# Kernel optimization log

Measured on AMD Instinct MI355X. Metric: run time of the kernel, lower is better.

Reference implementation:

```python
import jax, jax.numpy as jnp
import numpy as np

B, S, E = 16, 2048, 1024

def setup_inputs() -> dict:
    key = jax.random.key(0)
    ks = jax.random.split(key, 7)
    scale = 1.0 / np.sqrt(E)
    x = jax.random.normal(ks[0], (B, S, E), dtype=jnp.float32)
    wq = jax.random.normal(ks[1], (E, E), dtype=jnp.float32) * scale
    bq = jax.random.normal(ks[2], (E,), dtype=jnp.float32) * 0.01
    wk = jax.random.normal(ks[3], (E, E), dtype=jnp.float32) * scale
    bk = jax.random.normal(ks[4], (E,), dtype=jnp.float32) * 0.01
    wv = jax.random.normal(ks[5], (E, E), dtype=jnp.float32) * scale
    bv = jax.random.normal(ks[6], (E,), dtype=jnp.float32) * 0.01
    return {"x": x, "wq": wq, "bq": bq, "wk": wk, "bk": bk, "wv": wv, "bv": bv}

def reference(x, wq, bq, wk, bk, wv, bv):
    # Linear layers: y = x @ W^T + b (torch nn.Linear convention)
    Q = jnp.einsum('bse,fe->bsf', x, wq) + bq
    K = jnp.einsum('bse,fe->bsf', x, wk) + bk
    V = jnp.einsum('bse,fe->bsf', x, wv) + bv
    scale = 1.0 / jnp.sqrt(jnp.asarray(x.shape[-1], dtype=x.dtype))
    score = jnp.einsum('bqe,bke->bqk', Q, K) * scale  # [B,S,S]
    attn = jax.nn.softmax(score, axis=-1)
    # dropout is identity in eval mode
    context = jnp.einsum('bqk,bke->bqe', attn, V)  # [B,S,E]
    return jnp.mean(context, axis=1)  # [B,E]
```

## Files before the change

### kernel.cpp

```cpp
#include <hip/hip_runtime.h>


#define B_ 16
#define S_ 2048
#define E_ 1024

typedef __bf16 bf16x8 __attribute__((ext_vector_type(8)));
typedef float f32x4 __attribute__((ext_vector_type(4)));

__device__ __forceinline__ unsigned short f2bf(float f) {
  unsigned int u = __float_as_uint(f);
  u = (u + 0x7FFFu + ((u >> 16) & 1u)) >> 16;
  return (unsigned short)u;
}
__device__ __forceinline__ float bf2f(unsigned short u) {
  return __uint_as_float((unsigned int)u << 16);
}

__global__ __launch_bounds__(256) void gvec_kernel(
    const float* __restrict__ wk, const float* __restrict__ bq,
    float* __restrict__ g) {
  const int e = blockIdx.x * 256 + threadIdx.x;
  const int f0 = blockIdx.y * 32;
  float acc = 0.f;
#pragma unroll
  for (int i = 0; i < 32; ++i) acc += wk[(size_t)(f0 + i) * E_ + e] * bq[f0 + i];
  atomicAdd(&g[e], acc);
}

__global__ __launch_bounds__(256) void cast_x_v_kernel(
    const float* __restrict__ x, const float* __restrict__ g,
    unsigned short* __restrict__ xbf, float* __restrict__ vs) {
  const int row = blockIdx.x, t = threadIdx.x;
  const size_t i = (size_t)row * E_ + t * 4;
  float4 v = *(const float4*)(x + i);
  float4 gv = *(const float4*)(g + t * 4);
  ushort4 o;
  o.x = f2bf(v.x); o.y = f2bf(v.y); o.z = f2bf(v.z); o.w = f2bf(v.w);
  *(ushort4*)(xbf + i) = o;
  float p = v.x * gv.x + v.y * gv.y + v.z * gv.z + v.w * gv.w;
#pragma unroll
  for (int off = 32; off >= 1; off >>= 1) p += __shfl_xor(p, off);
  __shared__ float wsp[4];
  if ((t & 63) == 0) wsp[t >> 6] = p;
  __syncthreads();
  if (t == 0) vs[row] = (wsp[0] + wsp[1] + wsp[2] + wsp[3]) * 0.03125f;
}

__global__ __launch_bounds__(256) void tcast_kernel(
    const float* __restrict__ src, unsigned short* __restrict__ dst) {
  __shared__ float tile[32][33];
  const int tx = threadIdx.x & 31, ty = threadIdx.x >> 5;
  const int f0 = blockIdx.y * 32, e0 = blockIdx.x * 32;
#pragma unroll
  for (int j = 0; j < 4; ++j)
    tile[ty + 8 * j][tx] = src[(size_t)(f0 + ty + 8 * j) * E_ + e0 + tx];
  __syncthreads();
#pragma unroll
  for (int j = 0; j < 4; ++j)
    dst[(size_t)(e0 + ty + 8 * j) * E_ + f0 + tx] = f2bf(tile[tx][ty + 8 * j]);
}

template <int MODE>
__global__ __launch_bounds__(256, 2) void gemm_bt(
    const unsigned short* __restrict__ A, const unsigned short* __restrict__ Bm,
    unsigned short* __restrict__ Cout, const float* __restrict__ bias,
    float* __restrict__ rowsum, float scale,
    int K, int lda, int ldb, int ldc,
    long long strideA, long long strideB, long long strideC) {
  __shared__ unsigned short As[128 * 64];
  __shared__ unsigned short Bs[128 * 64];

  const int tid = threadIdx.x;
  const int wave = tid >> 6;
  const int lane = tid & 63;
  const int bz = blockIdx.z;
  const unsigned short* Ab = A + (size_t)bz * strideA;
  const unsigned short* Bb = Bm + (size_t)bz * strideB;
  const int rowBase = blockIdx.y * 128;
  const int colBase = blockIdx.x * 128;

  const int waveM = wave >> 1, waveN = wave & 1;
  const int lrow = lane & 15, lq = lane >> 4;

  const int rsub = lane >> 3;
  const int gOff = (((lane & 7) ^ rsub) << 3);

  f32x4 acc[4][4];
#pragma unroll
  for (int i = 0; i < 4; ++i)
#pragma unroll
    for (int j = 0; j < 4; ++j) {
      f32x4 z = {0.f, 0.f, 0.f, 0.f};
      acc[i][j] = z;
    }

  for (int k0 = 0; k0 < K; k0 += 64) {
#pragma unroll
    for (int i = 0; i < 4; ++i) {
      const int chunk = wave * 4 + i;
      const int r = chunk * 8 + rsub;
      const unsigned short* ga = Ab + (size_t)(rowBase + r) * lda + (k0 + gOff);
      const unsigned short* gb = Bb + (size_t)(colBase + r) * ldb + (k0 + gOff);
      __builtin_amdgcn_global_load_lds(
          (const __attribute__((address_space(1))) void*)ga,
          (__attribute__((address_space(3))) void*)(&As[chunk * 512]), 16, 0, 0);
      __builtin_amdgcn_global_load_lds(
          (const __attribute__((address_space(1))) void*)gb,
          (__attribute__((address_space(3))) void*)(&Bs[chunk * 512]), 16, 0, 0);
    }
    __syncthreads();

#pragma unroll
    for (int ks = 0; ks < 2; ++ks) {
      const int gg = (((ks * 4 + lq) ^ (lrow & 7)) << 3);
      bf16x8 af[4], bfv[4];
#pragma unroll
      for (int mi = 0; mi < 4; ++mi)
        af[mi] = *(const bf16x8*)(&As[(waveM * 64 + mi * 16 + lrow) * 64 + gg]);
#pragma unroll
      for (int ni = 0; ni < 4; ++ni)
        bfv[ni] = *(const bf16x8*)(&Bs[(waveN * 64 + ni * 16 + lrow) * 64 + gg]);
#pragma unroll
      for (int mi = 0; mi < 4; ++mi)
#pragma unroll
        for (int ni = 0; ni < 4; ++ni)
          acc[mi][ni] = __builtin_amdgcn_mfma_f32_16x16x32_bf16(
              af[mi], bfv[ni], acc[mi][ni], 0, 0, 0);
    }
    __syncthreads();
  }

  unsigned short* Cb = Cout + (size_t)bz * strideC;
  if constexpr (MODE == 0) {
#pragma unroll
    for (int mi = 0; mi < 4; ++mi) {
      const int grow = rowBase + waveM * 64 + mi * 16 + lq * 4;
#pragma unroll
      for (int ni = 0; ni < 4; ++ni) {
        const int gcol = colBase + waveN * 64 + ni * 16 + lrow;
        const float badd = bias ? bias[gcol] : 0.f;
#pragma unroll
        for (int r = 0; r < 4; ++r)
          Cb[(size_t)(grow + r) * ldc + gcol] =
              f2bf(acc[mi][ni][r] * scale + badd);
      }
    }
  } else {
    float* rs = rowsum + (size_t)bz * S_;
    const float* vsb = bias + (size_t)bz * S_;
#pragma unroll
    for (int mi = 0; mi < 4; ++mi) {
      const int grow = rowBase + waveM * 64 + mi * 16 + lq * 4;
#pragma unroll
      for (int r = 0; r < 4; ++r) {
        float partial = 0.f;
#pragma unroll
        for (int ni = 0; ni < 4; ++ni) {
          const int gcol = colBase + waveN * 64 + ni * 16 + lrow;
          const float e = __expf(acc[mi][ni][r] * scale + vsb[gcol]);
          Cb[(size_t)(grow + r) * ldc + gcol] = f2bf(e);
          partial += e;
        }
        partial += __shfl_xor(partial, 1);
        partial += __shfl_xor(partial, 2);
        partial += __shfl_xor(partial, 4);
        partial += __shfl_xor(partial, 8);
        if (lrow == 0) atomicAdd(&rs[grow + r], partial);
      }
    }
  }
}

__global__ __launch_bounds__(256) void colsum_kernel(
    const unsigned int* __restrict__ Epk, const float* __restrict__ rowsum,
    float* __restrict__ wsum) {
  const int b = blockIdx.y, q0 = blockIdx.x * 128, t = threadIdx.x;
  __shared__ float rinv[128];
  if (t < 128) rinv[t] = 1.0f / rowsum[(size_t)b * S_ + q0 + t];
  __syncthreads();
  float cs0[4] = {0, 0, 0, 0}, cs1[4] = {0, 0, 0, 0};
  const unsigned int* Eb = Epk + ((size_t)b * S_ + q0) * (S_ / 2);
  for (int q = 0; q < 128; ++q) {
    const float rv = rinv[q];
    const unsigned int* row = Eb + (size_t)q * (S_ / 2);
#pragma unroll
    for (int j = 0; j < 4; ++j) {
      const unsigned int p = row[t + 256 * j];
      cs0[j] += bf2f((unsigned short)(p & 0xFFFF)) * rv;
      cs1[j] += bf2f((unsigned short)(p >> 16)) * rv;
    }
  }
  const float inv = 1.0f / (float)S_;
#pragma unroll
  for (int j = 0; j < 4; ++j) {
    atomicAdd(&wsum[(size_t)b * S_ + 2 * (t + 256 * j)], cs0[j] * inv);
    atomicAdd(&wsum[(size_t)b * S_ + 2 * (t + 256 * j) + 1], cs1[j] * inv);
  }
}

__global__ __launch_bounds__(256) void xbar_kernel(
    const float* __restrict__ x, const float* __restrict__ wsum,
    float* __restrict__ xbar) {
  const int b = blockIdx.y, kc = blockIdx.x, t = threadIdx.x;
  float acc[4] = {0, 0, 0, 0};
  for (int k0 = 0; k0 < 256; ++k0) {
    const int k = kc * 256 + k0;
    const float w = wsum[(size_t)b * S_ + k];
    const float* xr = x + ((size_t)b * S_ + k) * E_;
#pragma unroll
    for (int c = 0; c < 4; ++c) acc[c] += w * xr[c * 256 + t];
  }
#pragma unroll
  for (int c = 0; c < 4; ++c)
    atomicAdd(&xbar[(size_t)b * E_ + c * 256 + t], acc[c]);
}

__global__ __launch_bounds__(256) void out_kernel(
    const float* __restrict__ xbar, const float* __restrict__ wv,
    const float* __restrict__ bv, float* __restrict__ out) {
  const int gid = blockIdx.x * 256 + threadIdx.x;
  const int b = gid >> 10, e = gid & 1023;
  const float4* xr = (const float4*)(xbar + (size_t)b * E_);
  const float4* wr = (const float4*)(wv + (size_t)e * E_);
  float s = 0.f;
  for (int j = 0; j < E_ / 4; ++j) {
    float4 a = xr[j], w = wr[j];
    s += a.x * w.x + a.y * w.y + a.z * w.z + a.w * w.w;
  }
  out[gid] = s + bv[e];
}

extern "C" void kernel_launch(void* const* d_in, const int* in_sizes, int n_in,
                              void* d_out, int out_size, void* d_ws,
                              size_t ws_size, hipStream_t stream) {
  const float* x = (const float*)d_in[0];
  const float* wq = (const float*)d_in[1];
  const float* bq = (const float*)d_in[2];
  const float* wk = (const float*)d_in[3];
  const float* wv = (const float*)d_in[5];
  const float* bv = (const float*)d_in[6];
  float* out = (float*)d_out;

  char* ws = (char*)d_ws;
  const size_t MB = 1ull << 20;
  unsigned short* xbf = (unsigned short*)(ws);
  unsigned short* y = (unsigned short*)(ws + 64 * MB);
  unsigned short* Ebuf = (unsigned short*)(ws + 128 * MB);
  unsigned short* WqT = (unsigned short*)(ws + 256 * MB);
  unsigned short* WkT = (unsigned short*)(ws + 258 * MB);
  unsigned short* Mt = (unsigned short*)(ws + 260 * MB);
  float* g = (float*)(ws + 262 * MB);
  float* rowsum = g + E_;
  float* wsum = rowsum + B_ * S_;
  float* xbar = wsum + B_ * S_;
  float* vs = xbar + B_ * E_;

  hipMemsetAsync(g, 0, (size_t)(E_ + 2 * B_ * S_ + B_ * E_) * sizeof(float),
                 stream);

  gvec_kernel<<<dim3(E_ / 256, 32), 256, 0, stream>>>(wk, bq, g);
  cast_x_v_kernel<<<B_ * S_, 256, 0, stream>>>(x, g, xbf, vs);
  tcast_kernel<<<dim3(32, 32), 256, 0, stream>>>(wq, WqT);
  tcast_kernel<<<dim3(32, 32), 256, 0, stream>>>(wk, WkT);

  gemm_bt<0><<<dim3(8, 8), 256, 0, stream>>>(
      WkT, WqT, Mt, nullptr, nullptr, 1.0f, E_, E_, E_, E_, 0, 0, 0);
  gemm_bt<0><<<dim3(E_ / 128, (B_ * S_) / 128), 256, 0, stream>>>(
      xbf, Mt, y, nullptr, nullptr, 1.0f, E_, E_, E_, E_, 0, 0, 0);
  gemm_bt<1><<<dim3(S_ / 128, S_ / 128, B_), 256, 0, stream>>>(
      y, xbf, Ebuf, vs, rowsum, 0.03125f, E_, E_, E_, S_,
      (long long)S_ * E_, (long long)S_ * E_, (long long)S_ * S_);

  colsum_kernel<<<dim3(S_ / 128, B_), 256, 0, stream>>>(
      (const unsigned int*)Ebuf, rowsum, wsum);
  xbar_kernel<<<dim3(S_ / 256, B_), 256, 0, stream>>>(x, wsum, xbar);
  out_kernel<<<(B_ * E_) / 256, 256, 0, stream>>>(xbar, wv, bv, out);
}
```

Measured before the change: 580.3 us.

## Store softmax exponentials as packed fp8 and split xbar/out reductions wider

The unnormalized attention exponentials are now stored as fp8 (packed four per 32-bit word, with a permuted column order) instead of bf16. This halves the 64 MB-per-batch E buffer traffic written by the score GEMM and read by the column-sum kernel, and the column-sum indexing is changed to match the new packing. The xbar kernel now uses float4 loads and more blocks. The output GEMV is split over four K-chunks using atomics on a zeroed output. The fp8 format risks accuracy loss in the attention weights, and the extra atomics add contention.

```diff
diff --git a/kernel.cpp b/kernel.cpp
--- a/kernel.cpp
+++ b/kernel.cpp
@@ -7,14 +7,12 @@
 
 typedef __bf16 bf16x8 __attribute__((ext_vector_type(8)));
 typedef float f32x4 __attribute__((ext_vector_type(4)));
+typedef float f32x2 __attribute__((ext_vector_type(2)));
 
 __device__ __forceinline__ unsigned short f2bf(float f) {
   unsigned int u = __float_as_uint(f);
   u = (u + 0x7FFFu + ((u >> 16) & 1u)) >> 16;
   return (unsigned short)u;
-}
-__device__ __forceinline__ float bf2f(unsigned short u) {
-  return __uint_as_float((unsigned int)u << 16);
 }
 
 __global__ __launch_bounds__(256) void gvec_kernel(
@@ -64,7 +62,7 @@
 template <int MODE>
 __global__ __launch_bounds__(256, 2) void gemm_bt(
     const unsigned short* __restrict__ A, const unsigned short* __restrict__ Bm,
-    unsigned short* __restrict__ Cout, const float* __restrict__ bias,
+    void* __restrict__ Cout, const float* __restrict__ bias,
     float* __restrict__ rowsum, float scale,
     int K, int lda, int ldb, int ldc,
     long long strideA, long long strideB, long long strideC) {
@@ -131,8 +129,8 @@
     __syncthreads();
   }
 
-  unsigned short* Cb = Cout + (size_t)bz * strideC;
   if constexpr (MODE == 0) {
+    unsigned short* Cb = (unsigned short*)Cout + (size_t)bz * strideC;
 #pragma unroll
     for (int mi = 0; mi < 4; ++mi) {
       const int grow = rowBase + waveM * 64 + mi * 16 + lq * 4;
@@ -147,21 +145,30 @@
       }
     }
   } else {
+    unsigned char* Eb = (unsigned char*)Cout + (size_t)bz * strideC;
     float* rs = rowsum + (size_t)bz * S_;
     const float* vsb = bias + (size_t)bz * S_;
+    float badd[4];
+#pragma unroll
+    for (int ni = 0; ni < 4; ++ni)
+      badd[ni] = vsb[colBase + waveN * 64 + ni * 16 + lrow];
 #pragma unroll
     for (int mi = 0; mi < 4; ++mi) {
       const int grow = rowBase + waveM * 64 + mi * 16 + lq * 4;
 #pragma unroll
       for (int r = 0; r < 4; ++r) {
+        float e[4];
         float partial = 0.f;
 #pragma unroll
         for (int ni = 0; ni < 4; ++ni) {
-          const int gcol = colBase + waveN * 64 + ni * 16 + lrow;
-          const float e = __expf(acc[mi][ni][r] * scale + vsb[gcol]);
-          Cb[(size_t)(grow + r) * ldc + gcol] = f2bf(e);
-          partial += e;
+          e[ni] = __expf(acc[mi][ni][r] * scale + badd[ni]);
+          partial += e[ni];
         }
+        unsigned int pk = 0;
+        pk = __builtin_amdgcn_cvt_pk_fp8_f32(e[0], e[1], pk, false);
+        pk = __builtin_amdgcn_cvt_pk_fp8_f32(e[2], e[3], pk, true);
+        *(unsigned int*)(&Eb[(size_t)(grow + r) * S_ + colBase + waveN * 64 +
+                             lrow * 4]) = pk;
         partial += __shfl_xor(partial, 1);
         partial += __shfl_xor(partial, 2);
         partial += __shfl_xor(partial, 4);
@@ -175,27 +182,34 @@
 __global__ __launch_bounds__(256) void colsum_kernel(
     const unsigned int* __restrict__ Epk, const float* __restrict__ rowsum,
     float* __restrict__ wsum) {
-  const int b = blockIdx.y, q0 = blockIdx.x * 128, t = threadIdx.x;
-  __shared__ float rinv[128];
-  if (t < 128) rinv[t] = 1.0f / rowsum[(size_t)b * S_ + q0 + t];
+  const int b = blockIdx.y, q0 = blockIdx.x * 64, t = threadIdx.x;
+  __shared__ float rinv[64];
+  if (t < 64) rinv[t] = 1.0f / rowsum[(size_t)b * S_ + q0 + t];
   __syncthreads();
-  float cs0[4] = {0, 0, 0, 0}, cs1[4] = {0, 0, 0, 0};
-  const unsigned int* Eb = Epk + ((size_t)b * S_ + q0) * (S_ / 2);
-  for (int q = 0; q < 128; ++q) {
+  float cs[2][4] = {{0, 0, 0, 0}, {0, 0, 0, 0}};
+  const unsigned int* Eb = Epk + ((size_t)b * S_ + q0) * (S_ / 4);
+  for (int q = 0; q < 64; ++q) {
     const float rv = rinv[q];
-    const unsigned int* row = Eb + (size_t)q * (S_ / 2);
-#pragma unroll
-    for (int j = 0; j < 4; ++j) {
+    const unsigned int* row = Eb + (size_t)q * (S_ / 4);
+#pragma unroll
+    for (int j = 0; j < 2; ++j) {
       const unsigned int p = row[t + 256 * j];
-      cs0[j] += bf2f((unsigned short)(p & 0xFFFF)) * rv;
-      cs1[j] += bf2f((unsigned short)(p >> 16)) * rv;
+      f32x2 lo = __builtin_amdgcn_cvt_pk_f32_fp8(p, false);
+      f32x2 hi = __builtin_amdgcn_cvt_pk_f32_fp8(p, true);
+      cs[j][0] += lo[0] * rv;
+      cs[j][1] += lo[1] * rv;
+      cs[j][2] += hi[0] * rv;
+      cs[j][3] += hi[1] * rv;
     }
   }
   const float inv = 1.0f / (float)S_;
 #pragma unroll
-  for (int j = 0; j < 4; ++j) {
-    atomicAdd(&wsum[(size_t)b * S_ + 2 * (t + 256 * j)], cs0[j] * inv);
-    atomicAdd(&wsum[(size_t)b * S_ + 2 * (t + 256 * j) + 1], cs1[j] * inv);
+  for (int j = 0; j < 2; ++j) {
+    const int d = t + 256 * j;
+    const int base = (d >> 4) * 64 + (d & 15);
+#pragma unroll
+    for (int jj = 0; jj < 4; ++jj)
+      atomicAdd(&wsum[(size_t)b * S_ + base + 16 * jj], cs[j][jj] * inv);
   }
 }
 
@@ -203,17 +217,19 @@
     const float* __restrict__ x, const float* __restrict__ wsum,
     float* __restrict__ xbar) {
   const int b = blockIdx.y, kc = blockIdx.x, t = threadIdx.x;
-  float acc[4] = {0, 0, 0, 0};
-  for (int k0 = 0; k0 < 256; ++k0) {
-    const int k = kc * 256 + k0;
+  float4 acc = {0.f, 0.f, 0.f, 0.f};
+  for (int k0 = 0; k0 < 128; ++k0) {
+    const int k = kc * 128 + k0;
     const float w = wsum[(size_t)b * S_ + k];
-    const float* xr = x + ((size_t)b * S_ + k) * E_;
-#pragma unroll
-    for (int c = 0; c < 4; ++c) acc[c] += w * xr[c * 256 + t];
-  }
-#pragma unroll
-  for (int c = 0; c < 4; ++c)
-    atomicAdd(&xbar[(size_t)b * E_ + c * 256 + t], acc[c]);
+    const float4 xv = *(const float4*)(x + ((size_t)b * S_ + k) * E_ + t * 4);
+    acc.x += w * xv.x; acc.y += w * xv.y;
+    acc.z += w * xv.z; acc.w += w * xv.w;
+  }
+  float* xb = xbar + (size_t)b * E_ + t * 4;
+  atomicAdd(&xb[0], acc.x);
+  atomicAdd(&xb[1], acc.y);
+  atomicAdd(&xb[2], acc.z);
+  atomicAdd(&xb[3], acc.w);
 }
 
 __global__ __launch_bounds__(256) void out_kernel(
@@ -221,14 +237,16 @@
     const float* __restrict__ bv, float* __restrict__ out) {
   const int gid = blockIdx.x * 256 + threadIdx.x;
   const int b = gid >> 10, e = gid & 1023;
-  const float4* xr = (const float4*)(xbar + (size_t)b * E_);
-  const float4* wr = (const float4*)(wv + (size_t)e * E_);
+  const int c0 = blockIdx.y * 64;
+  const float4* xr = (const float4*)(xbar + (size_t)b * E_) + c0;
+  const float4* wr = (const float4*)(wv + (size_t)e * E_) + c0;
   float s = 0.f;
-  for (int j = 0; j < E_ / 4; ++j) {
+  for (int j = 0; j < 64; ++j) {
     float4 a = xr[j], w = wr[j];
     s += a.x * w.x + a.y * w.y + a.z * w.z + a.w * w.w;
   }
-  out[gid] = s + bv[e];
+  if (blockIdx.y == 0) s += bv[e];
+  atomicAdd(&out[gid], s);
 }
 
 extern "C" void kernel_launch(void* const* d_in, const int* in_sizes, int n_in,
@@ -246,11 +264,11 @@
   const size_t MB = 1ull << 20;
   unsigned short* xbf = (unsigned short*)(ws);
   unsigned short* y = (unsigned short*)(ws + 64 * MB);
-  unsigned short* Ebuf = (unsigned short*)(ws + 128 * MB);
-  unsigned short* WqT = (unsigned short*)(ws + 256 * MB);
-  unsigned short* WkT = (unsigned short*)(ws + 258 * MB);
-  unsigned short* Mt = (unsigned short*)(ws + 260 * MB);
-  float* g = (float*)(ws + 262 * MB);
+  unsigned char* Ebuf = (unsigned char*)(ws + 128 * MB);
+  unsigned short* WqT = (unsigned short*)(ws + 192 * MB);
+  unsigned short* WkT = (unsigned short*)(ws + 194 * MB);
+  unsigned short* Mt = (unsigned short*)(ws + 196 * MB);
+  float* g = (float*)(ws + 198 * MB);
   float* rowsum = g + E_;
   float* wsum = rowsum + B_ * S_;
   float* xbar = wsum + B_ * S_;
@@ -258,6 +276,7 @@
 
   hipMemsetAsync(g, 0, (size_t)(E_ + 2 * B_ * S_ + B_ * E_) * sizeof(float),
                  stream);
+  hipMemsetAsync(out, 0, (size_t)B_ * E_ * sizeof(float), stream);
 
   gvec_kernel<<<dim3(E_ / 256, 32), 256, 0, stream>>>(wk, bq, g);
   cast_x_v_kernel<<<B_ * S_, 256, 0, stream>>>(x, g, xbf, vs);
@@ -265,15 +284,15 @@
   tcast_kernel<<<dim3(32, 32), 256, 0, stream>>>(wk, WkT);
 
   gemm_bt<0><<<dim3(8, 8), 256, 0, stream>>>(
-      WkT, WqT, Mt, nullptr, nullptr, 1.0f, E_, E_, E_, E_, 0, 0, 0);
+      WkT, WqT, (void*)Mt, nullptr, nullptr, 1.0f, E_, E_, E_, E_, 0, 0, 0);
   gemm_bt<0><<<dim3(E_ / 128, (B_ * S_) / 128), 256, 0, stream>>>(
-      xbf, Mt, y, nullptr, nullptr, 1.0f, E_, E_, E_, E_, 0, 0, 0);
+      xbf, Mt, (void*)y, nullptr, nullptr, 1.0f, E_, E_, E_, E_, 0, 0, 0);
   gemm_bt<1><<<dim3(S_ / 128, S_ / 128, B_), 256, 0, stream>>>(
-      y, xbf, Ebuf, vs, rowsum, 0.03125f, E_, E_, E_, S_,
+      y, xbf, (void*)Ebuf, vs, rowsum, 0.03125f, E_, E_, E_, S_,
       (long long)S_ * E_, (long long)S_ * E_, (long long)S_ * S_);
 
-  colsum_kernel<<<dim3(S_ / 128, B_), 256, 0, stream>>>(
+  colsum_kernel<<<dim3(S_ / 64, B_), 256, 0, stream>>>(
       (const unsigned int*)Ebuf, rowsum, wsum);
-  xbar_kernel<<<dim3(S_ / 256, B_), 256, 0, stream>>>(x, wsum, xbar);
-  out_kernel<<<(B_ * E_) / 256, 256, 0, stream>>>(xbar, wv, bv, out);
-}
+  xbar_kernel<<<dim3(16, B_), 256, 0, stream>>>(x, wsum, xbar);
+  out_kernel<<<dim3(B_ * E_ / 256, 4), 256, 0, stream>>>(xbar, wv, bv, out);
+}
```

Measured after the change: 512.0 us. 11.8% less time.
